# Kernel tuning notes

Measured on AMD Instinct MI355X. Metric: run time of the kernel, lower is better.

The kernel has to match this reference:

```python
import jax, jax.numpy as jnp
import numpy as np

B = 8          # graphs in batch
N = 10000      # nodes per graph
DEG = 16       # avg degree
F_IN = 128
H = 128
OUT = 64
RATIO = 0.5


def setup_inputs() -> dict:
    key = jax.random.key(0)
    ks = jax.random.split(key, 20)
    E = B * N * DEG
    x = jax.random.normal(ks[0], (B * N, F_IN), jnp.float32)
    gid = (jnp.arange(E, dtype=jnp.int32) // (N * DEG)) * N  # per-graph node offset
    src = jax.random.randint(ks[1], (E,), 0, N, jnp.int32) + gid
    dst = jax.random.randint(ks[2], (E,), 0, N, jnp.int32) + gid
    edge_index = jnp.stack([src, dst])

    def lin(k, fo, fi):
        return jax.random.normal(k, (fo, fi), jnp.float32) / np.sqrt(fi)

    return {
        "x": x,
        "edge_index": edge_index,
        "w1l_W": lin(ks[3], H, F_IN), "w1l_b": jnp.zeros((H,), jnp.float32),
        "w1r_W": lin(ks[4], H, F_IN),
        "pool1_w": jax.random.normal(ks[5], (H,), jnp.float32) / np.sqrt(H),
        "w2l_W": lin(ks[6], H, H), "w2l_b": jnp.zeros((H,), jnp.float32),
        "w2r_W": lin(ks[7], H, H),
        "pool2_w": jax.random.normal(ks[8], (H,), jnp.float32) / np.sqrt(H),
        "w3l_W": lin(ks[9], H, H), "w3l_b": jnp.zeros((H,), jnp.float32),
        "w3r_W": lin(ks[10], H, H),
        "pool3_w": jax.random.normal(ks[11], (H,), jnp.float32) / np.sqrt(H),
        "out_W": lin(ks[12], OUT, 2 * H), "out_b": jnp.zeros((OUT,), jnp.float32),
    }


def sage(x, src, dst, mask, Wl, bl, Wr, n_nodes):
    # PyG SAGEConv (mean aggr): lin_l(mean_{j->i} x_j) + lin_r(x_i); lin_l has bias.
    m = mask.astype(x.dtype)
    msg = x[src] * m[:, None]                                   # [E, F]
    agg = jax.ops.segment_sum(msg, dst, num_segments=n_nodes)   # [n, F]
    deg = jax.ops.segment_sum(m, dst, num_segments=n_nodes)     # [n]
    agg = agg / jnp.maximum(deg, 1.0)[:, None]                  # mean; empty -> 0
    return agg @ Wl.T + bl + x @ Wr.T


def topk_pool(x, src, dst, mask, w, n_per):
    # PyG TopKPooling: score = tanh(x.w / ||w||); keep top ceil(ratio*n) per graph;
    # x_out = x[perm] * score[perm]; edges filtered to surviving endpoints (masked here).
    k = int(np.ceil(RATIO * n_per))
    s = jnp.tanh((x @ w) / jnp.linalg.norm(w)).reshape(B, n_per)
    vals, idx = jax.lax.top_k(s, k)                             # [B, k]
    perm = (idx + (jnp.arange(B) * n_per)[:, None]).reshape(-1)  # global node ids
    x_new = x[perm] * vals.reshape(-1)[:, None]
    node_map = jnp.full((B * n_per,), -1, jnp.int32).at[perm].set(
        jnp.arange(B * k, dtype=jnp.int32))
    ns, nd = node_map[src], node_map[dst]
    valid = mask & (ns >= 0) & (nd >= 0)
    return x_new, jnp.where(valid, ns, 0), jnp.where(valid, nd, 0), valid, k


def summarize(x, k):
    xr = x.reshape(B, k, -1)
    return jnp.concatenate([xr.mean(axis=1), xr.max(axis=1)], axis=1)  # [B, 2H]


def reference(x, edge_index, w1l_W, w1l_b, w1r_W, pool1_w,
              w2l_W, w2l_b, w2r_W, pool2_w,
              w3l_W, w3l_b, w3r_W, pool3_w, out_W, out_b):
    src, dst = edge_index[0], edge_index[1]
    mask = jnp.ones(src.shape, bool)

    x = sage(x, src, dst, mask, w1l_W, w1l_b, w1r_W, B * N)
    x, src, dst, mask, k1 = topk_pool(x, src, dst, mask, pool1_w, N)
    s1 = summarize(x, k1)

    x = jax.nn.relu(sage(x, src, dst, mask, w2l_W, w2l_b, w2r_W, B * k1))
    x, src, dst, mask, k2 = topk_pool(x, src, dst, mask, pool2_w, k1)
    s2 = summarize(x, k2)

    x = sage(x, src, dst, mask, w3l_W, w3l_b, w3r_W, B * k2)
    x, src, dst, mask, k3 = topk_pool(x, src, dst, mask, pool3_w, k2)
    s3 = summarize(x, k3)

    summary = s1 + s2 + s3
    return summary @ out_W.T + out_b
```

## Files before the change

kernel.cpp:

```cpp
#include <hip/hip_runtime.h>
#include <hip/hip_bf16.h>
#include <math.h>

constexpr int B    = 8;
constexpr int NPG  = 10000;
constexpr int F    = 128;
constexpr int OUTD = 64;
constexpr int E    = B * NPG * 16;
constexpr int N0   = B * NPG;
constexpr int K1   = 5000, K2 = 2500, K3 = 1250;
constexpr int N1   = B * K1;
constexpr int N2   = B * K2;
constexpr int N3   = B * K3;
constexpr int PSPLIT = 256;
constexpr int ESH  = E / 8;
constexpr int KCH  = 8;
constexpr int CH   = ESH / KCH;

constexpr size_t OFF_IN   = 0;
constexpr size_t SZ_IN    = (size_t)N0 * 256 / 2;
constexpr size_t OFF_HB   = OFF_IN + SZ_IN;
constexpr size_t SZ_HB    = (size_t)N0 * F / 2;
constexpr size_t OFF_SC   = OFF_HB + SZ_HB;
constexpr size_t OFF_KEY  = OFF_SC + N0;
constexpr size_t OFF_MAP  = OFF_KEY + N0;
constexpr size_t OFF_MAP2 = OFF_MAP + N0;
constexpr size_t OFF_SEL1 = OFF_MAP2 + N1;
constexpr size_t OFF_SEL2 = OFF_SEL1 + N1;
constexpr size_t OFF_SEL3 = OFF_SEL2 + N2;
constexpr size_t OFF_SOC  = OFF_SEL3 + N3;
constexpr size_t OFF_VAL  = OFF_SOC + N2;
constexpr size_t OFF_CSR  = OFF_VAL + N1;
constexpr size_t OFF_CNT  = OFF_CSR + E;
constexpr size_t OFF_CUR0 = OFF_CNT + (size_t)64 * NPG;
constexpr size_t OFF_HSUM = OFF_CUR0 + (size_t)64 * NPG;
constexpr size_t OFF_INCL = OFF_HSUM + N0;
constexpr size_t OFF_BSUM = OFF_INCL + N0;
constexpr size_t OFF_RS   = OFF_BSUM + 512;
constexpr size_t OFF_PART = OFF_RS + N0 + 64;
constexpr size_t OFF_SUM  = OFF_PART + (size_t)B * PSPLIT * 2 * F;
constexpr size_t OFF_WCAT = OFF_SUM + (size_t)B * 2 * F;
constexpr size_t OFF_MISC = OFF_WCAT + 3 * 128 * 256 / 2;

typedef __attribute__((ext_vector_type(8))) short short8;
typedef __attribute__((ext_vector_type(4))) float floatx4;

__device__ inline unsigned f2key(float f) {
    unsigned u = __float_as_uint(f);
    return (u & 0x80000000u) ? ~u : (u | 0x80000000u);
}
__device__ inline unsigned short f2b(float f) {
    unsigned u = __float_as_uint(f);
    return (unsigned short)((u + 0x7FFFu + ((u >> 16) & 1u)) >> 16);
}
__device__ inline float b2f(unsigned short u) {
    return __uint_as_float((unsigned)u << 16);
}

__global__ void k_prep3(const float* __restrict__ Wl1, const float* __restrict__ Wr1,
                        const float* __restrict__ Wl2, const float* __restrict__ Wr2,
                        const float* __restrict__ Wl3, const float* __restrict__ Wr3,
                        const float* __restrict__ p1, const float* __restrict__ p2,
                        const float* __restrict__ p3,
                        unsigned short* __restrict__ wcat, float* __restrict__ normv) {
    int b = blockIdx.x;
    if (b == 96) {
        int t = threadIdx.x;
        int which = t >> 6, lane = t & 63;
        if (which < 3) {
            const float* pw = (which == 0) ? p1 : (which == 1) ? p2 : p3;
            float v = 0.0f;
            for (int j = lane; j < F; j += 64) { float a = pw[j]; v += a * a; }
            for (int o = 32; o > 0; o >>= 1) v += __shfl_down(v, o);
            if (lane == 0) normv[which] = sqrtf(v);
        }
        return;
    }
    int stage = b >> 5;
    const float* Wl = (stage == 0) ? Wl1 : (stage == 1) ? Wl2 : Wl3;
    const float* Wr = (stage == 0) ? Wr1 : (stage == 1) ? Wr2 : Wr3;
    unsigned short* W = wcat + (size_t)stage * 128 * 256;
    int idx = ((b & 31) * 256 + threadIdx.x) * 4;
    int o = idx >> 8, k = idx & 255;
    const float* p = (k < 128) ? (Wl + o * 128 + k) : (Wr + o * 128 + (k - 128));
    float4 v = *(const float4*)p;
    ushort4 u;
    u.x = f2b(v.x); u.y = f2b(v.y); u.z = f2b(v.z); u.w = f2b(v.w);
    *(ushort4*)(W + idx) = u;
}

__global__ void k_cvt(const float* __restrict__ x, unsigned short* __restrict__ IN, int n) {
    long t = blockIdx.x * (long)blockDim.x + threadIdx.x;
    int i = (int)(t >> 5), lane = (int)(t & 31);
    if (i >= n) return;
    float4 v = ((const float4*)(x + (size_t)i * F))[lane];
    ushort4 u;
    u.x = f2b(v.x); u.y = f2b(v.y); u.z = f2b(v.z); u.w = f2b(v.w);
    *(ushort4*)(IN + (size_t)i * 256 + 128 + lane * 4) = u;
}

__global__ __launch_bounds__(1024) void k_hist_p(const int* __restrict__ dst,
                                                 int* __restrict__ cnt) {
    __shared__ int h[NPG];
    int b = blockIdx.x, g = b & 7, k = b >> 3;
    for (int i = threadIdx.x; i < NPG; i += 1024) h[i] = 0;
    __syncthreads();
    int base = g * ESH + k * CH;
    for (int i = threadIdx.x; i < CH; i += 1024) {
        int d = __builtin_nontemporal_load(dst + base + i) - g * NPG;
        atomicAdd(&h[d], 1);
    }
    __syncthreads();
    int* o = cnt + (size_t)(g * KCH + k) * NPG;
    for (int i = threadIdx.x; i < NPG; i += 1024) o[i] = h[i];
}

__global__ void k_sumcnt(const int* __restrict__ cnt, int* __restrict__ hsum) {
    int i = blockIdx.x * blockDim.x + threadIdx.x;
    if (i >= N0) return;
    int g = i / NPG, l = i - g * NPG;
    const int* c = cnt + (size_t)g * KCH * NPG + l;
    int t = 0;
#pragma unroll
    for (int k = 0; k < KCH; k++) t += c[(size_t)k * NPG];
    hsum[i] = t;
}

__global__ __launch_bounds__(256) void k_scan1(const int* __restrict__ in, int n,
                                               int* __restrict__ incl, int* __restrict__ bsum) {
    __shared__ int s[256];
    int i = blockIdx.x * 256 + threadIdx.x;
    int v = (i < n) ? in[i] : 0;
    s[threadIdx.x] = v;
    __syncthreads();
    for (int off = 1; off < 256; off <<= 1) {
        int t = s[threadIdx.x] + ((threadIdx.x >= off) ? s[threadIdx.x - off] : 0);
        __syncthreads();
        s[threadIdx.x] = t;
        __syncthreads();
    }
    if (i < n) incl[i] = s[threadIdx.x];
    if (threadIdx.x == 255) bsum[blockIdx.x] = s[255];
}

__global__ __launch_bounds__(512) void k_scan2(int* __restrict__ bsum, int nb) {
    __shared__ int s[512];
    int t = threadIdx.x;
    int v = (t < nb) ? bsum[t] : 0;
    s[t] = v;
    __syncthreads();
    for (int off = 1; off < 512; off <<= 1) {
        int u = s[t] + ((t >= off) ? s[t - off] : 0);
        __syncthreads();
        s[t] = u;
        __syncthreads();
    }
    if (t < nb) bsum[t] = s[t] - v;
}

__global__ void k_scan3c(const int* __restrict__ in, const int* __restrict__ incl,
                         const int* __restrict__ bsum, const int* __restrict__ cnt,
                         int* __restrict__ rowstart, int* __restrict__ cur0) {
    int i = blockIdx.x * 256 + threadIdx.x;
    if (i >= N0) return;
    int ex = incl[i] - in[i] + bsum[blockIdx.x];
    rowstart[i] = ex;
    if (i == N0 - 1) rowstart[N0] = ex + in[i];
    int g = i / NPG, l = i - g * NPG;
    const int* c = cnt + (size_t)g * KCH * NPG + l;
    int* u = cur0 + (size_t)g * KCH * NPG + l;
    int run = ex;
#pragma unroll
    for (int k = 0; k < KCH; k++) {
        u[(size_t)k * NPG] = run;
        run += c[(size_t)k * NPG];
    }
}

__global__ __launch_bounds__(1024) void k_csr_p(const int* __restrict__ src,
                                                const int* __restrict__ dst,
                                                const int* __restrict__ cur0,
                                                int* __restrict__ csr) {
    __shared__ int h[NPG];
    int b = blockIdx.x, g = b & 7, k = b >> 3;
    const int* u = cur0 + (size_t)(g * KCH + k) * NPG;
    for (int i = threadIdx.x; i < NPG; i += 1024) h[i] = u[i];
    __syncthreads();
    int base = g * ESH + k * CH;
    for (int i = threadIdx.x; i < CH; i += 1024) {
        int d = __builtin_nontemporal_load(dst + base + i) - g * NPG;
        int s = __builtin_nontemporal_load(src + base + i);
        int p = atomicAdd(&h[d], 1);
        csr[p] = s;
    }
}

__global__ void k_composechain(int* __restrict__ m1, const int* __restrict__ m2,
                               const int* __restrict__ s2, const int* __restrict__ s1,
                               int* __restrict__ soc, int n1, int n2) {
    int i = blockIdx.x * blockDim.x + threadIdx.x;
    if (i < n2) soc[i] = s1[s2[i]];
    if (i < n1) { int a = m1[i]; m1[i] = (a >= 0) ? m2[a] : -1; }
}

__global__ __launch_bounds__(256) void k_agg2b(unsigned short* __restrict__ IN,
                                               const int* __restrict__ rowstart,
                                               const int* __restrict__ csr, int npg) {
    int g = blockIdx.x & 7;
    int local = (blockIdx.x >> 3) * 8 + (threadIdx.x >> 5);
    int lane = threadIdx.x & 31;
    if (local >= npg) return;
    int i = g * npg + local;
    int b = rowstart[i], e = rowstart[i + 1];
    float a0 = 0, a1 = 0, a2 = 0, a3 = 0;
    int j = b;
    for (; j + 4 <= e; j += 4) {
        int s0 = __builtin_nontemporal_load(csr + j);
        int s1 = __builtin_nontemporal_load(csr + j + 1);
        int s2 = __builtin_nontemporal_load(csr + j + 2);
        int s3 = __builtin_nontemporal_load(csr + j + 3);
        ushort4 u0 = *(const ushort4*)(IN + (size_t)s0 * 256 + 128 + lane * 4);
        ushort4 u1 = *(const ushort4*)(IN + (size_t)s1 * 256 + 128 + lane * 4);
        ushort4 u2 = *(const ushort4*)(IN + (size_t)s2 * 256 + 128 + lane * 4);
        ushort4 u3 = *(const ushort4*)(IN + (size_t)s3 * 256 + 128 + lane * 4);
        a0 += (b2f(u0.x) + b2f(u1.x)) + (b2f(u2.x) + b2f(u3.x));
        a1 += (b2f(u0.y) + b2f(u1.y)) + (b2f(u2.y) + b2f(u3.y));
        a2 += (b2f(u0.z) + b2f(u1.z)) + (b2f(u2.z) + b2f(u3.z));
        a3 += (b2f(u0.w) + b2f(u1.w)) + (b2f(u2.w) + b2f(u3.w));
    }
    for (; j < e; j++) {
        int s0 = __builtin_nontemporal_load(csr + j);
        ushort4 u0 = *(const ushort4*)(IN + (size_t)s0 * 256 + 128 + lane * 4);
        a0 += b2f(u0.x); a1 += b2f(u0.y); a2 += b2f(u0.z); a3 += b2f(u0.w);
    }
    float rd = 1.0f / fmaxf((float)(e - b), 1.0f);
    ushort4 o;
    o.x = f2b(a0 * rd); o.y = f2b(a1 * rd); o.z = f2b(a2 * rd); o.w = f2b(a3 * rd);
    *(ushort4*)(IN + (size_t)i * 256 + lane * 4) = o;
}

__global__ __launch_bounds__(256) void k_agg2m(unsigned short* __restrict__ IN,
                                               const int* __restrict__ rowstart,
                                               const int* __restrict__ csr,
                                               const int* __restrict__ map,
                                               const int* __restrict__ orig_of, int npg) {
    int g = blockIdx.x & 7;
    int local = (blockIdx.x >> 3) * 8 + (threadIdx.x >> 5);
    int lane = threadIdx.x & 31;
    if (local >= npg) return;
    int i = g * npg + local;
    int o = orig_of[i];
    int b = rowstart[o], e = rowstart[o + 1];
    float a0 = 0, a1 = 0, a2 = 0, a3 = 0;
    int d = 0;
    int j = b;
    for (; j + 2 <= e; j += 2) {
        int c0 = __builtin_nontemporal_load(csr + j);
        int c1 = __builtin_nontemporal_load(csr + j + 1);
        int s0 = map[c0], s1 = map[c1];
        if (s0 >= 0) {
            ushort4 u = *(const ushort4*)(IN + (size_t)s0 * 256 + 128 + lane * 4);
            a0 += b2f(u.x); a1 += b2f(u.y); a2 += b2f(u.z); a3 += b2f(u.w);
            d++;
        }
        if (s1 >= 0) {
            ushort4 u = *(const ushort4*)(IN + (size_t)s1 * 256 + 128 + lane * 4);
            a0 += b2f(u.x); a1 += b2f(u.y); a2 += b2f(u.z); a3 += b2f(u.w);
            d++;
        }
    }
    if (j < e) {
        int c0 = __builtin_nontemporal_load(csr + j);
        int s0 = map[c0];
        if (s0 >= 0) {
            ushort4 u = *(const ushort4*)(IN + (size_t)s0 * 256 + 128 + lane * 4);
            a0 += b2f(u.x); a1 += b2f(u.y); a2 += b2f(u.z); a3 += b2f(u.w);
            d++;
        }
    }
    float rd = 1.0f / fmaxf((float)d, 1.0f);
    ushort4 out;
    out.x = f2b(a0 * rd); out.y = f2b(a1 * rd); out.z = f2b(a2 * rd); out.w = f2b(a3 * rd);
    *(ushort4*)(IN + (size_t)i * 256 + lane * 4) = out;
}

__global__ __launch_bounds__(256) void k_sage_b(
    const unsigned short* __restrict__ IN, const unsigned short* __restrict__ Wcat,
    const float* __restrict__ bias, const float* __restrict__ poolw,
    const float* __restrict__ normv,
    unsigned short* __restrict__ hb, float* __restrict__ sc,
    unsigned* __restrict__ key, int npg, int relu) {
    __shared__ float lds[64][132];
    int tid = threadIdx.x;
    int wid = tid >> 6, lane = tid & 63;
    int q = lane >> 4, l15 = lane & 15;
    int g = blockIdx.x & 7, lb = blockIdx.x >> 3;
    int gbase = g * npg;
    int rowloc0 = lb * 128 + wid * 32;

    floatx4 acc0[8], acc1[8];
#pragma unroll
    for (int c = 0; c < 8; c++) {
        acc0[c] = (floatx4){0.f, 0.f, 0.f, 0.f};
        acc1[c] = (floatx4){0.f, 0.f, 0.f, 0.f};
    }

    const unsigned short* bbase = Wcat + (size_t)l15 * 256 + q * 8;
    int lr0 = min(rowloc0 + l15, npg - 1);
    int lr1 = min(rowloc0 + 16 + l15, npg - 1);
    const unsigned short* a0p = IN + (size_t)(gbase + lr0) * 256 + q * 8;
    const unsigned short* a1p = IN + (size_t)(gbase + lr1) * 256 + q * 8;
#pragma unroll
    for (int ks = 0; ks < 8; ks++) {
        short8 a0 = *(const short8*)(a0p + (ks << 5));
        short8 a1 = *(const short8*)(a1p + (ks << 5));
#pragma unroll
        for (int c = 0; c < 8; c++) {
            short8 b = *(const short8*)(bbase + (c << 12) + (ks << 5));
            acc0[c] = __builtin_amdgcn_mfma_f32_16x16x32_bf16(a0, b, acc0[c], 0, 0, 0);
            acc1[c] = __builtin_amdgcn_mfma_f32_16x16x32_bf16(a1, b, acc1[c], 0, 0, 0);
        }
    }

    float invn = 1.0f / (*normv);
#pragma unroll
    for (int t = 0; t < 2; t++) {
        float p0 = 0, p1 = 0, p2 = 0, p3 = 0;
#pragma unroll
        for (int c = 0; c < 8; c++) {
            int col = (c << 4) + l15;
            float bv = bias[col];
            float wv = poolw[col];
            floatx4 v = (t == 0) ? acc0[c] : acc1[c];
            v[0] += bv; v[1] += bv; v[2] += bv; v[3] += bv;
            if (relu) {
                v[0] = fmaxf(v[0], 0.f); v[1] = fmaxf(v[1], 0.f);
                v[2] = fmaxf(v[2], 0.f); v[3] = fmaxf(v[3], 0.f);
            }
            p0 += v[0] * wv; p1 += v[1] * wv; p2 += v[2] * wv; p3 += v[3] * wv;
            int lr = wid * 16 + q * 4;
            lds[lr + 0][col] = v[0];
            lds[lr + 1][col] = v[1];
            lds[lr + 2][col] = v[2];
            lds[lr + 3][col] = v[3];
        }
#pragma unroll
        for (int off = 1; off < 16; off <<= 1) {
            p0 += __shfl_xor(p0, off);
            p1 += __shfl_xor(p1, off);
            p2 += __shfl_xor(p2, off);
            p3 += __shfl_xor(p3, off);
        }
        if (l15 == 0) {
            float ps[4] = {p0, p1, p2, p3};
#pragma unroll
            for (int j = 0; j < 4; j++) {
                int lrow = rowloc0 + t * 16 + q * 4 + j;
                if (lrow < npg) {
                    float s = tanhf(ps[j] * invn);
                    sc[gbase + lrow] = s;
                    key[gbase + lrow] = f2key(s);
                }
            }
        }
        __syncthreads();
#pragma unroll
        for (int it = 0; it < 4; it++) {
            int task = it * 256 + tid;
            int r = task >> 4, grp = task & 15;
            int lrow = lb * 128 + (r >> 4) * 32 + t * 16 + (r & 15);
            if (lrow < npg) {
                float4 lo = *(const float4*)&lds[r][grp * 8];
                float4 hi = *(const float4*)&lds[r][grp * 8 + 4];
                short8 u;
                u[0] = (short)f2b(lo.x); u[1] = (short)f2b(lo.y);
                u[2] = (short)f2b(lo.z); u[3] = (short)f2b(lo.w);
                u[4] = (short)f2b(hi.x); u[5] = (short)f2b(hi.y);
                u[6] = (short)f2b(hi.z); u[7] = (short)f2b(hi.w);
                *(short8*)(hb + (size_t)(gbase + lrow) * 128 + grp * 8) = u;
            }
        }
        __syncthreads();
    }
}

__global__ __launch_bounds__(1024) void k_topk(
    const unsigned* __restrict__ keys, const float* __restrict__ sc,
    int n_per, int k,
    int* __restrict__ node_map, int* __restrict__ sel_old, float* __restrict__ vals) {
    int g = blockIdx.x, tid = threadIdx.x;
    int lane = tid & 63, wid = tid >> 6;
    const unsigned* kk = keys + (size_t)g * n_per;
    const float* ss = sc + (size_t)g * n_per;
    __shared__ int hist[256];
    __shared__ int suf[256];
    __shared__ unsigned sprefix;
    __shared__ int sr, sfound;
    __shared__ int we2[16], ws2[16];
    __shared__ int carry_pos, carry_eq;
    if (tid == 0) { sprefix = 0; sr = k; carry_pos = 0; carry_eq = 0; }
    __syncthreads();

    for (int b = 3; b >= 0; b--) {
        if (tid < 256) hist[tid] = 0;
        __syncthreads();
        unsigned pfx = sprefix;
        unsigned maskhi = (b == 3) ? 0u : (0xFFFFFFFFu << ((b + 1) * 8));
        for (int i = tid * 4; i < n_per; i += 4096) {
            uint4 kv4 = *(const uint4*)(kk + i);
#pragma unroll
            for (int j = 0; j < 4; j++) {
                unsigned kv = (j == 0) ? kv4.x : (j == 1) ? kv4.y : (j == 2) ? kv4.z : kv4.w;
                if ((kv & maskhi) == (pfx & maskhi))
                    atomicAdd(&hist[(kv >> (b * 8)) & 255], 1);
            }
        }
        __syncthreads();
        if (tid < 256) suf[tid] = hist[tid];
        __syncthreads();
        for (int off = 1; off < 256; off <<= 1) {
            int t = 0;
            if (tid < 256) t = suf[tid] + ((tid + off < 256) ? suf[tid + off] : 0);
            __syncthreads();
            if (tid < 256) suf[tid] = t;
            __syncthreads();
        }
        int r = sr;
        if (tid < 256) {
            int hi = (tid == 255) ? 0 : suf[tid + 1];
            if (hi < r && suf[tid] >= r) sfound = tid;
        }
        __syncthreads();
        if (tid == 0) {
            int v = sfound;
            int hi = (v == 255) ? 0 : suf[v + 1];
            sr = r - hi;
            sprefix = pfx | ((unsigned)v << (b * 8));
        }
        __syncthreads();
    }
    unsigned K = sprefix;
    int need = sr;
    __syncthreads();

    int nch = (n_per + 1023) >> 10;
    for (int ch = 0; ch < nch; ch++) {
        int i = (ch << 10) + tid;
        int valid = (i < n_per);
        unsigned kv = valid ? kk[i] : 0u;
        int is_gt = valid && (kv > K);
        int is_eq = valid && (kv == K);
        int e_incl = is_eq;
#pragma unroll
        for (int off = 1; off < 64; off <<= 1) {
            int t = __shfl_up(e_incl, off);
            e_incl += (lane >= off) ? t : 0;
        }
        if (lane == 63) we2[wid] = e_incl;
        __syncthreads();
        if (tid < 16) {
            int v = we2[tid];
#pragma unroll
            for (int off = 1; off < 16; off <<= 1) {
                int t = __shfl_up(v, off);
                v += ((int)tid >= off) ? t : 0;
            }
            we2[tid] = v;
        }
        __syncthreads();
        int eq_before = carry_eq + (e_incl - is_eq) + (wid ? we2[wid - 1] : 0);
        int sel = is_gt || (is_eq && eq_before < need);
        int s_incl = sel;
#pragma unroll
        for (int off = 1; off < 64; off <<= 1) {
            int t = __shfl_up(s_incl, off);
            s_incl += (lane >= off) ? t : 0;
        }
        if (lane == 63) ws2[wid] = s_incl;
        __syncthreads();
        if (tid < 16) {
            int v = ws2[tid];
#pragma unroll
            for (int off = 1; off < 16; off <<= 1) {
                int t = __shfl_up(v, off);
                v += ((int)tid >= off) ? t : 0;
            }
            ws2[tid] = v;
        }
        __syncthreads();
        int pos = carry_pos + (s_incl - sel) + (wid ? ws2[wid - 1] : 0);
        if (valid) {
            if (sel) {
                int ni = g * k + pos;
                node_map[(size_t)g * n_per + i] = ni;
                sel_old[ni] = g * n_per + i;
                vals[ni] = ss[i];
            } else {
                node_map[(size_t)g * n_per + i] = -1;
            }
        }
        __syncthreads();
        if (tid == 0) { carry_pos += ws2[15]; carry_eq += we2[15]; }
        __syncthreads();
    }
}

__global__ void k_gatherb(const unsigned short* __restrict__ hb,
                          const int* __restrict__ sel_old,
                          const float* __restrict__ vals,
                          unsigned short* __restrict__ INnext, int m) {
    long t = blockIdx.x * (long)blockDim.x + threadIdx.x;
    int i = (int)(t >> 5), lane = (int)(t & 31);
    if (i >= m) return;
    int oi = sel_old[i];
    float v = vals[i];
    ushort4 u = *(const ushort4*)(hb + (size_t)oi * 128 + lane * 4);
    ushort4 o;
    o.x = f2b(b2f(u.x) * v); o.y = f2b(b2f(u.y) * v);
    o.z = f2b(b2f(u.z) * v); o.w = f2b(b2f(u.w) * v);
    *(ushort4*)(INnext + (size_t)i * 256 + 128 + lane * 4) = o;
}

__global__ __launch_bounds__(64) void k_partial2(const unsigned short* __restrict__ IN,
                                                 int k, float* __restrict__ part) {
    int g = blockIdx.x >> 8, s = blockIdx.x & (PSPLIT - 1);
    int lane = threadIdx.x;
    int rows = (k + PSPLIT - 1) / PSPLIT;
    int r0 = s * rows, r1 = min(k, r0 + rows);
    float s0 = 0, s1 = 0, m0 = -INFINITY, m1 = -INFINITY;
    for (int r = r0; r < r1; r++) {
        ushort2 u = *(const ushort2*)(IN + (size_t)(g * k + r) * 256 + 128 + lane * 2);
        float v0 = b2f(u.x), v1 = b2f(u.y);
        s0 += v0; s1 += v1;
        m0 = fmaxf(m0, v0); m1 = fmaxf(m1, v1);
    }
    size_t base = ((size_t)(g * PSPLIT + s) * 2) * F;
    *(float2*)&part[base + lane * 2] = make_float2(s0, s1);
    *(float2*)&part[base + F + lane * 2] = make_float2(m0, m1);
}

__global__ __launch_bounds__(256) void k_sumreduce2(const float* __restrict__ part, int k,
                                                    float* __restrict__ summary, int accum) {
    int g = blockIdx.x;
    int half = threadIdx.x >> 7, f = threadIdx.x & 127;
    float sum = 0.0f, mx = -INFINITY;
    for (int s = 0; s < PSPLIT; s++) {
        float v = part[((size_t)(g * PSPLIT + s) * 2 + half) * F + f];
        sum += v;
        mx = fmaxf(mx, v);
    }
    float res = half ? mx : (sum / (float)k);
    int idx = g * 2 * F + half * F + f;
    if (accum) summary[idx] += res; else summary[idx] = res;
}

__global__ void k_out(const float* __restrict__ summary, const float* __restrict__ W,
                      const float* __restrict__ bias, float* __restrict__ out) {
    int g = blockIdx.x, j = threadIdx.x;
    float acc = bias[j];
    for (int t = 0; t < 2 * F; t++) acc += summary[g * 2 * F + t] * W[j * 2 * F + t];
    out[g * OUTD + j] = acc;
}

static inline int cdiv(long a, long b) { return (int)((a + b - 1) / b); }

extern "C" void kernel_launch(void* const* d_in, const int* in_sizes, int n_in,
                              void* d_out, int out_size, void* d_ws, size_t ws_size,
                              hipStream_t stream) {
    const float* x_in = (const float*)d_in[0];
    const int* ei     = (const int*)d_in[1];
    const float* w1lW = (const float*)d_in[2];
    const float* w1lb = (const float*)d_in[3];
    const float* w1rW = (const float*)d_in[4];
    const float* p1w  = (const float*)d_in[5];
    const float* w2lW = (const float*)d_in[6];
    const float* w2lb = (const float*)d_in[7];
    const float* w2rW = (const float*)d_in[8];
    const float* p2w  = (const float*)d_in[9];
    const float* w3lW = (const float*)d_in[10];
    const float* w3lb = (const float*)d_in[11];
    const float* w3rW = (const float*)d_in[12];
    const float* p3w  = (const float*)d_in[13];
    const float* outW = (const float*)d_in[14];
    const float* outb = (const float*)d_in[15];
    float* out = (float*)d_out;

    float* ws = (float*)d_ws;
    unsigned short* INb  = (unsigned short*)(ws + OFF_IN);
    unsigned short* hb   = (unsigned short*)(ws + OFF_HB);
    float* sc    = ws + OFF_SC;
    unsigned* key = (unsigned*)(ws + OFF_KEY);
    int* nmap1   = (int*)(ws + OFF_MAP);
    int* nmap2   = (int*)(ws + OFF_MAP2);
    int* selo1   = (int*)(ws + OFF_SEL1);
    int* selo2   = (int*)(ws + OFF_SEL2);
    int* selo3   = (int*)(ws + OFF_SEL3);
    int* soc     = (int*)(ws + OFF_SOC);
    float* vals  = ws + OFF_VAL;
    int* csr     = (int*)(ws + OFF_CSR);
    int* cnt     = (int*)(ws + OFF_CNT);
    int* cur0    = (int*)(ws + OFF_CUR0);
    int* hsum    = (int*)(ws + OFF_HSUM);
    int* incl    = (int*)(ws + OFF_INCL);
    int* bsum    = (int*)(ws + OFF_BSUM);
    int* rs      = (int*)(ws + OFF_RS);
    float* part    = ws + OFF_PART;
    float* summary = ws + OFF_SUM;
    unsigned short* wcat = (unsigned short*)(ws + OFF_WCAT);
    int* misc_i  = (int*)(ws + OFF_MISC);
    float* normv = (float*)(misc_i + 20);

    const int* esrc = ei;
    const int* edst = ei + E;

    {
        int n = N0, nb = cdiv(n, 256);
        k_prep3<<<97, 256, 0, stream>>>(w1lW, w1rW, w2lW, w2rW, w3lW, w3rW,
                                        p1w, p2w, p3w, wcat, normv);
        k_cvt<<<cdiv((long)n * 32, 256), 256, 0, stream>>>(x_in, INb, n);
        k_hist_p<<<64, 1024, 0, stream>>>(edst, cnt);
        k_sumcnt<<<nb, 256, 0, stream>>>(cnt, hsum);
        k_scan1<<<nb, 256, 0, stream>>>(hsum, n, incl, bsum);
        k_scan2<<<1, 512, 0, stream>>>(bsum, nb);
        k_scan3c<<<nb, 256, 0, stream>>>(hsum, incl, bsum, cnt, rs, cur0);
        k_csr_p<<<64, 1024, 0, stream>>>(esrc, edst, cur0, csr);
        k_agg2b<<<8 * cdiv(NPG, 8), 256, 0, stream>>>(INb, rs, csr, NPG);
        k_sage_b<<<8 * cdiv(NPG, 128), 256, 0, stream>>>(INb, wcat, w1lb, p1w, normv,
                                                         hb, sc, key, NPG, 0);
        k_topk<<<B, 1024, 0, stream>>>(key, sc, NPG, K1, nmap1, selo1, vals);
        k_gatherb<<<cdiv((long)N1 * 32, 256), 256, 0, stream>>>(hb, selo1, vals, INb, N1);
        k_partial2<<<B * PSPLIT, 64, 0, stream>>>(INb, K1, part);
        k_sumreduce2<<<B, 256, 0, stream>>>(part, K1, summary, 0);
    }

    {
        k_agg2m<<<8 * cdiv(K1, 8), 256, 0, stream>>>(INb, rs, csr, nmap1, selo1, K1);
        k_sage_b<<<8 * cdiv(K1, 128), 256, 0, stream>>>(INb, wcat + 32768, w2lb, p2w, normv + 1,
                                                        hb, sc, key, K1, 1);
        k_topk<<<B, 1024, 0, stream>>>(key, sc, K1, K2, nmap2, selo2, vals);
        k_gatherb<<<cdiv((long)N2 * 32, 256), 256, 0, stream>>>(hb, selo2, vals, INb, N2);
        k_partial2<<<B * PSPLIT, 64, 0, stream>>>(INb, K2, part);
        k_sumreduce2<<<B, 256, 0, stream>>>(part, K2, summary, 1);
        k_composechain<<<cdiv(N0, 256), 256, 0, stream>>>(nmap1, nmap2, selo2, selo1, soc, N0, N2);
    }

    {
        k_agg2m<<<8 * cdiv(K2, 8), 256, 0, stream>>>(INb, rs, csr, nmap1, soc, K2);
        k_sage_b<<<8 * cdiv(K2, 128), 256, 0, stream>>>(INb, wcat + 65536, w3lb, p3w, normv + 2,
                                                        hb, sc, key, K2, 0);
        k_topk<<<B, 1024, 0, stream>>>(key, sc, K2, K3, nmap2, selo3, vals);
        k_gatherb<<<cdiv((long)N3 * 32, 256), 256, 0, stream>>>(hb, selo3, vals, INb, N3);
        k_partial2<<<B * PSPLIT, 64, 0, stream>>>(INb, K3, part);
        k_sumreduce2<<<B, 256, 0, stream>>>(part, K3, summary, 1);
    }

    k_out<<<B, OUTD, 0, stream>>>(summary, outW, outb, out);
}
```

Baseline: 415.4 us.

## Split CSR histogram into more chunks and unroll neighbor gather loops deeper

New measurement: 379.2 us. 1.1x faster.

```diff
diff --git a/kernel.cpp b/kernel.cpp
--- a/kernel.cpp
+++ b/kernel.cpp
@@ -14,7 +14,7 @@
 constexpr int N3   = B * K3;
 constexpr int PSPLIT = 256;
 constexpr int ESH  = E / 8;
-constexpr int KCH  = 8;
+constexpr int KCH  = 32;
 constexpr int CH   = ESH / KCH;
 
 constexpr size_t OFF_IN   = 0;
@@ -31,9 +31,7 @@
 constexpr size_t OFF_SOC  = OFF_SEL3 + N3;
 constexpr size_t OFF_VAL  = OFF_SOC + N2;
 constexpr size_t OFF_CSR  = OFF_VAL + N1;
-constexpr size_t OFF_CNT  = OFF_CSR + E;
-constexpr size_t OFF_CUR0 = OFF_CNT + (size_t)64 * NPG;
-constexpr size_t OFF_HSUM = OFF_CUR0 + (size_t)64 * NPG;
+constexpr size_t OFF_HSUM = OFF_CSR + E;
 constexpr size_t OFF_INCL = OFF_HSUM + N0;
 constexpr size_t OFF_BSUM = OFF_INCL + N0;
 constexpr size_t OFF_RS   = OFF_BSUM + 512;
@@ -214,21 +212,29 @@
     int b = rowstart[i], e = rowstart[i + 1];
     float a0 = 0, a1 = 0, a2 = 0, a3 = 0;
     int j = b;
-    for (; j + 4 <= e; j += 4) {
+    for (; j + 8 <= e; j += 8) {
+        int sx[8];
+#pragma unroll
+        for (int t = 0; t < 8; t++) sx[t] = __builtin_nontemporal_load(csr + j + t);
+        ushort4 ux[8];
+#pragma unroll
+        for (int t = 0; t < 8; t++)
+            ux[t] = *(const ushort4*)(IN + (size_t)sx[t] * 256 + 128 + lane * 4);
+#pragma unroll
+        for (int t = 0; t < 8; t++) {
+            a0 += b2f(ux[t].x); a1 += b2f(ux[t].y);
+            a2 += b2f(ux[t].z); a3 += b2f(ux[t].w);
+        }
+    }
+    for (; j + 2 <= e; j += 2) {
         int s0 = __builtin_nontemporal_load(csr + j);
         int s1 = __builtin_nontemporal_load(csr + j + 1);
-        int s2 = __builtin_nontemporal_load(csr + j + 2);
-        int s3 = __builtin_nontemporal_load(csr + j + 3);
         ushort4 u0 = *(const ushort4*)(IN + (size_t)s0 * 256 + 128 + lane * 4);
         ushort4 u1 = *(const ushort4*)(IN + (size_t)s1 * 256 + 128 + lane * 4);
-        ushort4 u2 = *(const ushort4*)(IN + (size_t)s2 * 256 + 128 + lane * 4);
-        ushort4 u3 = *(const ushort4*)(IN + (size_t)s3 * 256 + 128 + lane * 4);
-        a0 += (b2f(u0.x) + b2f(u1.x)) + (b2f(u2.x) + b2f(u3.x));
-        a1 += (b2f(u0.y) + b2f(u1.y)) + (b2f(u2.y) + b2f(u3.y));
-        a2 += (b2f(u0.z) + b2f(u1.z)) + (b2f(u2.z) + b2f(u3.z));
-        a3 += (b2f(u0.w) + b2f(u1.w)) + (b2f(u2.w) + b2f(u3.w));
-    }
-    for (; j < e; j++) {
+        a0 += b2f(u0.x) + b2f(u1.x); a1 += b2f(u0.y) + b2f(u1.y);
+        a2 += b2f(u0.z) + b2f(u1.z); a3 += b2f(u0.w) + b2f(u1.w);
+    }
+    if (j < e) {
         int s0 = __builtin_nontemporal_load(csr + j);
         ushort4 u0 = *(const ushort4*)(IN + (size_t)s0 * 256 + 128 + lane * 4);
         a0 += b2f(u0.x); a1 += b2f(u0.y); a2 += b2f(u0.z); a3 += b2f(u0.w);
@@ -254,22 +260,23 @@
     float a0 = 0, a1 = 0, a2 = 0, a3 = 0;
     int d = 0;
     int j = b;
-    for (; j + 2 <= e; j += 2) {
+    for (; j + 4 <= e; j += 4) {
         int c0 = __builtin_nontemporal_load(csr + j);
         int c1 = __builtin_nontemporal_load(csr + j + 1);
-        int s0 = map[c0], s1 = map[c1];
-        if (s0 >= 0) {
-            ushort4 u = *(const ushort4*)(IN + (size_t)s0 * 256 + 128 + lane * 4);
-            a0 += b2f(u.x); a1 += b2f(u.y); a2 += b2f(u.z); a3 += b2f(u.w);
-            d++;
-        }
-        if (s1 >= 0) {
-            ushort4 u = *(const ushort4*)(IN + (size_t)s1 * 256 + 128 + lane * 4);
-            a0 += b2f(u.x); a1 += b2f(u.y); a2 += b2f(u.z); a3 += b2f(u.w);
-            d++;
-        }
-    }
-    if (j < e) {
+        int c2 = __builtin_nontemporal_load(csr + j + 2);
+        int c3 = __builtin_nontemporal_load(csr + j + 3);
+        int m0 = map[c0], m1 = map[c1], m2 = map[c2], m3 = map[c3];
+#pragma unroll
+        for (int t = 0; t < 4; t++) {
+            int s = (t == 0) ? m0 : (t == 1) ? m1 : (t == 2) ? m2 : m3;
+            if (s >= 0) {
+                ushort4 u = *(const ushort4*)(IN + (size_t)s * 256 + 128 + lane * 4);
+                a0 += b2f(u.x); a1 += b2f(u.y); a2 += b2f(u.z); a3 += b2f(u.w);
+                d++;
+            }
+        }
+    }
+    for (; j < e; j++) {
         int c0 = __builtin_nontemporal_load(csr + j);
         int s0 = map[c0];
         if (s0 >= 0) {
@@ -588,6 +595,8 @@
     float* ws = (float*)d_ws;
     unsigned short* INb  = (unsigned short*)(ws + OFF_IN);
     unsigned short* hb   = (unsigned short*)(ws + OFF_HB);
+    int* cnt     = (int*)(ws + OFF_HB);
+    int* cur0    = cnt + (size_t)B * KCH * NPG;
     float* sc    = ws + OFF_SC;
     unsigned* key = (unsigned*)(ws + OFF_KEY);
     int* nmap1   = (int*)(ws + OFF_MAP);
@@ -598,8 +607,6 @@
     int* soc     = (int*)(ws + OFF_SOC);
     float* vals  = ws + OFF_VAL;
     int* csr     = (int*)(ws + OFF_CSR);
-    int* cnt     = (int*)(ws + OFF_CNT);
-    int* cur0    = (int*)(ws + OFF_CUR0);
     int* hsum    = (int*)(ws + OFF_HSUM);
     int* incl    = (int*)(ws + OFF_INCL);
     int* bsum    = (int*)(ws + OFF_BSUM);
@@ -618,12 +625,12 @@
         k_prep3<<<97, 256, 0, stream>>>(w1lW, w1rW, w2lW, w2rW, w3lW, w3rW,
                                         p1w, p2w, p3w, wcat, normv);
         k_cvt<<<cdiv((long)n * 32, 256), 256, 0, stream>>>(x_in, INb, n);
-        k_hist_p<<<64, 1024, 0, stream>>>(edst, cnt);
+        k_hist_p<<<B * KCH, 1024, 0, stream>>>(edst, cnt);
         k_sumcnt<<<nb, 256, 0, stream>>>(cnt, hsum);
         k_scan1<<<nb, 256, 0, stream>>>(hsum, n, incl, bsum);
         k_scan2<<<1, 512, 0, stream>>>(bsum, nb);
         k_scan3c<<<nb, 256, 0, stream>>>(hsum, incl, bsum, cnt, rs, cur0);
-        k_csr_p<<<64, 1024, 0, stream>>>(esrc, edst, cur0, csr);
+        k_csr_p<<<B * KCH, 1024, 0, stream>>>(esrc, edst, cur0, csr);
         k_agg2b<<<8 * cdiv(NPG, 8), 256, 0, stream>>>(INb, rs, csr, NPG);
         k_sage_b<<<8 * cdiv(NPG, 128), 256, 0, stream>>>(INb, wcat, w1lb, p1w, normv,
                                                          hb, sc, key, NPG, 0);
```
